# Optimization experiments

Measured on AMD Instinct MI355X. Metric: run time of the kernel, lower is better.

The kernel has to match this reference:

```python
import jax, jax.numpy as jnp
import numpy as np

N, E, F_IN, H, L = 50000, 800000, 128, 256, 3


def setup_inputs() -> dict:
    key = jax.random.key(0)
    ks = jax.random.split(key, 6)
    s = 0.05  # keep activations well-scaled through 3 residual layers
    return {
        "x": jax.random.normal(ks[0], (N, F_IN), jnp.float32),
        "edge_index": jax.random.randint(ks[1], (2, E), 0, N, dtype=jnp.int32),
        "Wp": jax.random.normal(ks[2], (H, F_IN), jnp.float32) * s,
        "bp": jnp.zeros((H,), jnp.float32),
        "Wl": jax.random.normal(ks[3], (L, H, H), jnp.float32) * s,
        "bl": jnp.zeros((L, H), jnp.float32),
        "Wr": jax.random.normal(ks[4], (L, H, H), jnp.float32) * s,
        "gamma": jnp.ones((L, H), jnp.float32),
        "beta": jnp.zeros((L, H), jnp.float32),
    }


def _layernorm(x, g, b, eps=1e-5):
    mu = jnp.mean(x, axis=-1, keepdims=True)
    var = jnp.var(x, axis=-1, keepdims=True)
    return (x - mu) * jax.lax.rsqrt(var + eps) * g + b


def reference(x, edge_index, Wp, bp, Wl, bl, Wr, gamma, beta):
    n = x.shape[0]
    src, dst = edge_index[0], edge_index[1]
    # input projection + ReLU
    h = jax.nn.relu(x @ Wp.T + bp)  # [N, H]
    # mean-aggregation normalizer (PyG SAGEConv 'mean'): zero-degree nodes -> 0
    deg = jax.ops.segment_sum(jnp.ones_like(dst, jnp.float32), dst, num_segments=n)
    inv_deg = (1.0 / jnp.maximum(deg, 1.0))[:, None]  # [N, 1]
    num_layers = Wl.shape[0]
    for i in range(num_layers):
        res = h
        # SAGEConv: lin_l(mean of source-neighbor messages) + lin_r(self)
        agg = jax.ops.segment_sum(h[src], dst, num_segments=n) * inv_deg  # [N, H]
        h = agg @ Wl[i].T + bl[i] + h @ Wr[i].T
        # LayerNorm -> ReLU -> (dropout: eval-mode identity) -> residual
        h = jax.nn.relu(_layernorm(h, gamma[i], beta[i])) + res
    return h
```

## Files before the change

### kernel.cpp

```cpp
#include <hip/hip_runtime.h>

#define NN 50000
#define EE 800000
#define FIN 128
#define HH 256
#define NL 3

#define BM 64
#define BK 32
#define ABYTES (BM*BK*2)
#define BBYTES (HH*BK*2)
#define TILEB  (ABYTES + BBYTES)

typedef __bf16 bf16x8 __attribute__((ext_vector_type(8)));
typedef float  f32x4  __attribute__((ext_vector_type(4)));
typedef unsigned short u16x8 __attribute__((ext_vector_type(8)));

__device__ __forceinline__ float bf2f(unsigned short u){
    union { unsigned int i; float f; } v; v.i = ((unsigned int)u) << 16; return v.f;
}
__device__ __forceinline__ unsigned short f2bf(float f){
    union { float f; unsigned int i; } v; v.f = f;
    unsigned int r = v.i + 0x7FFF + ((v.i >> 16) & 1);
    return (unsigned short)(r >> 16);
}
__device__ __forceinline__ void gload16(const void* g, void* s){
    __builtin_amdgcn_global_load_lds(
        (const __attribute__((address_space(1))) void*)g,
        (__attribute__((address_space(3))) void*)s, 16, 0, 0);
}

__global__ void k_zero_i32(int* __restrict__ p, int n){
    int i = blockIdx.x*256 + threadIdx.x;
    if (i < n) p[i] = 0;
}
__global__ void k_count_deg(const int* __restrict__ dst, int* __restrict__ deg){
    int i = blockIdx.x*256 + threadIdx.x;
    if (i < EE) atomicAdd(&deg[dst[i]], 1);
}
__global__ void k_block_sum(const int* __restrict__ deg, int* __restrict__ bsum){
    __shared__ int s[1024];
    int i = blockIdx.x*1024 + threadIdx.x;
    s[threadIdx.x] = (i < NN) ? deg[i] : 0;
    __syncthreads();
    for (int o = 512; o > 0; o >>= 1){
        if (threadIdx.x < o) s[threadIdx.x] += s[threadIdx.x + o];
        __syncthreads();
    }
    if (threadIdx.x == 0) bsum[blockIdx.x] = s[0];
}
__global__ void k_scan_bsum(int* __restrict__ bsum, int nb){
    if (threadIdx.x == 0 && blockIdx.x == 0){
        int run = 0;
        for (int i = 0; i < nb; ++i){ int v = bsum[i]; bsum[i] = run; run += v; }
    }
}
__global__ void k_make_off(const int* __restrict__ deg, const int* __restrict__ bsum,
                           int* __restrict__ off, int* __restrict__ pos,
                           float* __restrict__ invd){
    __shared__ int s[1024];
    int t = threadIdx.x;
    int i = blockIdx.x*1024 + t;
    int v = (i < NN) ? deg[i] : 0;
    s[t] = v; __syncthreads();
    for (int o = 1; o < 1024; o <<= 1){
        int add = (t >= o) ? s[t - o] : 0;
        __syncthreads();
        s[t] += add;
        __syncthreads();
    }
    if (i < NN){
        int excl = s[t] - v + bsum[blockIdx.x];
        off[i] = excl; pos[i] = excl;
        invd[i] = 1.0f / fmaxf((float)v, 1.0f);
    }
}
__global__ void k_build_csr(const int* __restrict__ src, const int* __restrict__ dst,
                            int* __restrict__ pos, int* __restrict__ csr){
    int i = blockIdx.x*256 + threadIdx.x;
    if (i < EE){
        int p = atomicAdd(&pos[dst[i]], 1);
        csr[p] = src[i];
    }
}

__global__ void k_cast4(const float* __restrict__ in, unsigned short* __restrict__ ob, int n4){
    int i = blockIdx.x*256 + threadIdx.x;
    if (i < n4){
        float4 v = *(const float4*)&in[i*4];
        ushort4 o; o.x=f2bf(v.x); o.y=f2bf(v.y); o.z=f2bf(v.z); o.w=f2bf(v.w);
        *(ushort4*)&ob[i*4] = o;
    }
}
__global__ void k_cast_wcat(const float* __restrict__ Wl, const float* __restrict__ Wr,
                            unsigned short* __restrict__ Wb){
    int i = blockIdx.x*256 + threadIdx.x;
    if (i < NL*HH*2*HH){
        int k = i & 511; int n = (i >> 9) & 255; int lyr = i >> 17;
        float v = (k < HH) ? Wl[((size_t)(lyr*HH)+n)*HH + k]
                           : Wr[((size_t)(lyr*HH)+n)*HH + (k-HH)];
        Wb[i] = f2bf(v);
    }
}

__global__ __launch_bounds__(256) void k_aggregate_bf(
    const unsigned short* __restrict__ hb, const int* __restrict__ csr,
    const int* __restrict__ off, const int* __restrict__ deg,
    const float* __restrict__ invd, unsigned short* __restrict__ aggb)
{
    const int wave = threadIdx.x >> 6, lane = threadIdx.x & 63;
    const int node = blockIdx.x*4 + wave;
    if (node >= NN) return;
    const int o = off[node], d = deg[node];
    const int half = lane >> 5;
    const int fl   = lane & 31;

    float acc[8] = {};
    int j = 0;
    for (; j + 8 <= d; j += 8){
        int s0 = csr[o + j     + half];
        int s1 = csr[o + j + 2 + half];
        int s2 = csr[o + j + 4 + half];
        int s3 = csr[o + j + 6 + half];
        u16x8 v0 = *(const u16x8*)&hb[(size_t)s0*HH + fl*8];
        u16x8 v1 = *(const u16x8*)&hb[(size_t)s1*HH + fl*8];
        u16x8 v2 = *(const u16x8*)&hb[(size_t)s2*HH + fl*8];
        u16x8 v3 = *(const u16x8*)&hb[(size_t)s3*HH + fl*8];
        #pragma unroll
        for (int k = 0; k < 8; ++k)
            acc[k] += (bf2f(v0[k]) + bf2f(v1[k])) + (bf2f(v2[k]) + bf2f(v3[k]));
    }
    for (; j < d; j += 2){
        int idx = j + half;
        if (idx < d){
            int s = csr[o + idx];
            u16x8 v = *(const u16x8*)&hb[(size_t)s*HH + fl*8];
            #pragma unroll
            for (int k = 0; k < 8; ++k) acc[k] += bf2f(v[k]);
        }
    }
    #pragma unroll
    for (int k = 0; k < 8; ++k) acc[k] += __shfl_xor(acc[k], 32);

    if (half == 0){
        float id = invd[node];
        u16x8 r;
        #pragma unroll
        for (int k = 0; k < 8; ++k) r[k] = f2bf(acc[k]*id);
        *(u16x8*)&aggb[(size_t)node*HH + fl*8] = r;
    }
}

template<int EPI>
__global__ __launch_bounds__(256) void k_gemm_mfma(
    const unsigned short* __restrict__ A0, int lda0,
    const unsigned short* __restrict__ A1, int lda1,
    const unsigned short* __restrict__ Bt,
    const float* __restrict__ bias,
    const float* __restrict__ gamma, const float* __restrict__ beta,
    const unsigned short* __restrict__ resb,
    float* __restrict__ outf, unsigned short* __restrict__ outb,
    int K0, int KTOT)
{
    __shared__ char smem[2*TILEB];
    const int t  = threadIdx.x;
    const int w  = t >> 6, l = t & 63;
    const int lr = l & 15, lg = l >> 4;
    const int m0 = blockIdx.x * BM;

    const int pA   = w*1024 + l*16;
    const int rowA = pA >> 6;
    const int swzA = (pA & 63) ^ ((rowA & 6) << 3);
    int growA = m0 + rowA; if (growA > NN-1) growA = NN-1;
    const char* a0base = (const char*)(A0 + (size_t)growA*lda0) + swzA;
    const char* a1base = (const char*)(A1 + (size_t)growA*lda1) + swzA;
    const char* bbase[4];
    #pragma unroll
    for (int c = 0; c < 4; ++c){
        int p = (w*4 + c)*1024 + l*16;
        int n = p >> 6;
        int swz = (p & 63) ^ ((n & 6) << 3);
        bbase[c] = (const char*)(Bt + (size_t)n*KTOT) + swz;
    }

    f32x4 acc[4][4] = {};

    auto stage = [&](int s, int buf){
        const int k0 = s * BK;
        char* dst = smem + buf*TILEB;
        const char* gA = (k0 < K0) ? (a0base + (size_t)k0*2)
                                   : (a1base + (size_t)(k0 - K0)*2);
        gload16(gA, dst + w*1024);
        #pragma unroll
        for (int c = 0; c < 4; ++c)
            gload16(bbase[c] + (size_t)k0*2, dst + ABYTES + (w*4 + c)*1024);
    };

    const int nsteps = KTOT / BK;
    stage(0, 0);
    for (int s = 0; s < nsteps; ++s){
        const int cur = s & 1;
        if (s + 1 < nsteps){
            stage(s + 1, cur ^ 1);
            asm volatile("s_waitcnt vmcnt(5)" ::: "memory");
        } else {
            asm volatile("s_waitcnt vmcnt(0)" ::: "memory");
        }
        __builtin_amdgcn_s_barrier();
        __builtin_amdgcn_sched_barrier(0);

        const char* As = smem + cur*TILEB;
        const char* Bs = As + ABYTES;
        const int kb = lg * 16;
        const int sw = (lr & 6) << 3;
        bf16x8 af[4], bfr[4];
        #pragma unroll
        for (int m = 0; m < 4; ++m){
            int r = m*16 + lr;
            af[m] = *(const bf16x8*)(As + r*64 + (kb ^ sw));
        }
        #pragma unroll
        for (int n = 0; n < 4; ++n){
            int r = w*64 + n*16 + lr;
            bfr[n] = *(const bf16x8*)(Bs + r*64 + (kb ^ sw));
        }
        #pragma unroll
        for (int m = 0; m < 4; ++m)
            #pragma unroll
            for (int n = 0; n < 4; ++n)
                acc[m][n] = __builtin_amdgcn_mfma_f32_16x16x32_bf16(af[m], bfr[n], acc[m][n], 0, 0, 0);

        asm volatile("s_waitcnt lgkmcnt(0)" ::: "memory");
        __builtin_amdgcn_s_barrier();
    }

    float bcol[4], gcol[4], becol[4];
    #pragma unroll
    for (int n = 0; n < 4; ++n){
        int c = w*64 + n*16 + lr;
        bcol[n] = bias[c];
        if (EPI >= 1){ gcol[n] = gamma[c]; becol[n] = beta[c]; }
    }

    if (EPI == 0){
        #pragma unroll
        for (int m = 0; m < 4; ++m)
        #pragma unroll
        for (int reg = 0; reg < 4; ++reg){
            int R = m*16 + lg*4 + reg;
            int grow = m0 + R;
            if (grow >= NN) continue;
            #pragma unroll
            for (int n = 0; n < 4; ++n){
                int c = w*64 + n*16 + lr;
                float v = fmaxf(acc[m][n][reg] + bcol[n], 0.f);
                outb[(size_t)grow*HH + c] = f2bf(v);
            }
        }
    } else {
        float sm[4][4], sq[4][4];
        #pragma unroll
        for (int m = 0; m < 4; ++m)
        #pragma unroll
        for (int reg = 0; reg < 4; ++reg){
            float s = 0.f, q = 0.f;
            #pragma unroll
            for (int n = 0; n < 4; ++n){
                float v = acc[m][n][reg] + bcol[n];
                acc[m][n][reg] = v;
                s += v; q += v*v;
            }
            sm[m][reg] = s; sq[m][reg] = q;
        }
        #pragma unroll
        for (int mask = 1; mask <= 8; mask <<= 1){
            #pragma unroll
            for (int m = 0; m < 4; ++m)
            #pragma unroll
            for (int reg = 0; reg < 4; ++reg){
                sm[m][reg] += __shfl_xor(sm[m][reg], mask);
                sq[m][reg] += __shfl_xor(sq[m][reg], mask);
            }
        }
        float* red = (float*)smem;
        __syncthreads();
        if (lr == 0){
            #pragma unroll
            for (int m = 0; m < 4; ++m)
            #pragma unroll
            for (int reg = 0; reg < 4; ++reg){
                int R = m*16 + lg*4 + reg;
                red[(w*64 + R)*2 + 0] = sm[m][reg];
                red[(w*64 + R)*2 + 1] = sq[m][reg];
            }
        }
        __syncthreads();
        #pragma unroll
        for (int m = 0; m < 4; ++m)
        #pragma unroll
        for (int reg = 0; reg < 4; ++reg){
            int R = m*16 + lg*4 + reg;
            float S = 0.f, Q = 0.f;
            #pragma unroll
            for (int ww = 0; ww < 4; ++ww){
                S += red[(ww*64 + R)*2 + 0];
                Q += red[(ww*64 + R)*2 + 1];
            }
            float mean = S * (1.0f/HH);
            float var  = Q * (1.0f/HH) - mean*mean;
            float inv  = rsqrtf(var + 1e-5f);
            int grow = m0 + R;
            if (grow >= NN) continue;
            #pragma unroll
            for (int n = 0; n < 4; ++n){
                int c = w*64 + n*16 + lr;
                float o = fmaxf((acc[m][n][reg] - mean)*inv*gcol[n] + becol[n], 0.f)
                          + bf2f(resb[(size_t)grow*HH + c]);
                if (EPI == 1) outb[(size_t)grow*HH + c] = f2bf(o);
                else          outf[(size_t)grow*HH + c] = o;
            }
        }
    }
}

extern "C" void kernel_launch(void* const* d_in, const int* in_sizes, int n_in,
                              void* d_out, int out_size, void* d_ws, size_t ws_size,
                              hipStream_t stream) {
    const float* x     = (const float*)d_in[0];
    const int*   ei    = (const int*)d_in[1];
    const int*   srcI  = ei;
    const int*   dstI  = ei + EE;
    const float* Wp    = (const float*)d_in[2];
    const float* bp    = (const float*)d_in[3];
    const float* Wl    = (const float*)d_in[4];
    const float* bl    = (const float*)d_in[5];
    const float* Wr    = (const float*)d_in[6];
    const float* gamma = (const float*)d_in[7];
    const float* beta  = (const float*)d_in[8];
    float* out = (float*)d_out;

    char* ws = (char*)d_ws;
    size_t off_b = 0;
    auto alloc = [&](size_t bytes) -> char* {
        char* p = ws + off_b;
        off_b = (off_b + bytes + 255) & ~(size_t)255;
        return p;
    };
    unsigned short* Hb0  = (unsigned short*)alloc((size_t)NN*HH*2);
    unsigned short* Hb1  = (unsigned short*)alloc((size_t)NN*HH*2);
    unsigned short* AGGb = (unsigned short*)alloc((size_t)NN*HH*2);
    unsigned short* Xb   = AGGb;
    int*   csr  = (int*)alloc((size_t)EE*4);
    int*   deg  = (int*)alloc((size_t)NN*4);
    int*   offs = (int*)alloc((size_t)NN*4);
    int*   pos  = (int*)alloc((size_t)NN*4);
    float* invd = (float*)alloc((size_t)NN*4);
    int*   bsum = (int*)alloc(64*4);
    unsigned short* Wpb = (unsigned short*)alloc((size_t)HH*FIN*2);
    unsigned short* Wb  = (unsigned short*)alloc((size_t)NL*HH*2*HH*2);
    (void)ws_size; (void)in_sizes; (void)n_in; (void)out_size;

    const int NB = (NN + 1023)/1024;

    k_zero_i32<<<(NN + 255)/256, 256, 0, stream>>>(deg, NN);
    k_count_deg<<<(EE + 255)/256, 256, 0, stream>>>(dstI, deg);
    k_block_sum<<<NB, 1024, 0, stream>>>(deg, bsum);
    k_scan_bsum<<<1, 1, 0, stream>>>(bsum, NB);
    k_make_off<<<NB, 1024, 0, stream>>>(deg, bsum, offs, pos, invd);
    k_build_csr<<<(EE + 255)/256, 256, 0, stream>>>(srcI, dstI, pos, csr);

    k_cast4<<<(NN*FIN/4 + 255)/256, 256, 0, stream>>>(x, Xb, NN*FIN/4);
    k_cast4<<<(HH*FIN/4 + 255)/256, 256, 0, stream>>>(Wp, Wpb, HH*FIN/4);
    k_cast_wcat<<<(NL*HH*2*HH + 255)/256, 256, 0, stream>>>(Wl, Wr, Wb);

    const int GB = (NN + BM - 1)/BM;

    k_gemm_mfma<0><<<GB, 256, 0, stream>>>(Xb, FIN, Xb, FIN, Wpb, bp,
                                           nullptr, nullptr, nullptr,
                                           nullptr, Hb0, FIN, FIN);

    unsigned short* hin = Hb0;
    for (int lyr = 0; lyr < NL; ++lyr){
        k_aggregate_bf<<<(NN + 3)/4, 256, 0, stream>>>(hin, csr, offs, deg, invd, AGGb);
        unsigned short* hout = (hin == Hb0) ? Hb1 : Hb0;
        const unsigned short* Wbt = Wb + (size_t)lyr*HH*2*HH;
        if (lyr < NL-1)
            k_gemm_mfma<1><<<GB, 256, 0, stream>>>(AGGb, HH, hin, HH, Wbt, bl + lyr*HH,
                                                   gamma + lyr*HH, beta + lyr*HH, hin,
                                                   nullptr, hout, HH, 2*HH);
        else
            k_gemm_mfma<2><<<GB, 256, 0, stream>>>(AGGb, HH, hin, HH, Wbt, bl + lyr*HH,
                                                   gamma + lyr*HH, beta + lyr*HH, hin,
                                                   out, nullptr, HH, 2*HH);
        hin = hout;
    }
}
```

Before: 421.1 us.

## Fuse neighbor mean-aggregation into the SAGE layer GEMM via shared memory

Removes the standalone aggregation kernel and computes the mean-aggregated rows for each 64-row tile directly inside the GEMM. The results are written into a swizzled LDS buffer that serves as the first half of the A operand. This avoids writing and re-reading the aggregated bf16 matrix in global memory for each layer and saves one launch per layer. In exchange, LDS use per block grows, which may lower occupancy. The latency-bound gather now runs with far fewer concurrent waves, each handling 16 nodes one after another.

New measurement: 570.1 us. 1.35x slower.

```diff
diff --git a/kernel.cpp b/kernel.cpp
--- a/kernel.cpp
+++ b/kernel.cpp
@@ -8,9 +8,6 @@
 
 #define BM 64
 #define BK 32
-#define ABYTES (BM*BK*2)
-#define BBYTES (HH*BK*2)
-#define TILEB  (ABYTES + BBYTES)
 
 typedef __bf16 bf16x8 __attribute__((ext_vector_type(8)));
 typedef float  f32x4  __attribute__((ext_vector_type(4)));
@@ -29,6 +26,9 @@
         (const __attribute__((address_space(1))) void*)g,
         (__attribute__((address_space(3))) void*)s, 16, 0, 0);
 }
+#define WAITV4 asm volatile("s_waitcnt vmcnt(4)" ::: "memory")
+#define WAITV5 asm volatile("s_waitcnt vmcnt(5)" ::: "memory")
+#define WAITV0 asm volatile("s_waitcnt vmcnt(0)" ::: "memory")
 
 __global__ void k_zero_i32(int* __restrict__ p, int n){
     int i = blockIdx.x*256 + threadIdx.x;
@@ -103,55 +103,7 @@
     }
 }
 
-__global__ __launch_bounds__(256) void k_aggregate_bf(
-    const unsigned short* __restrict__ hb, const int* __restrict__ csr,
-    const int* __restrict__ off, const int* __restrict__ deg,
-    const float* __restrict__ invd, unsigned short* __restrict__ aggb)
-{
-    const int wave = threadIdx.x >> 6, lane = threadIdx.x & 63;
-    const int node = blockIdx.x*4 + wave;
-    if (node >= NN) return;
-    const int o = off[node], d = deg[node];
-    const int half = lane >> 5;
-    const int fl   = lane & 31;
-
-    float acc[8] = {};
-    int j = 0;
-    for (; j + 8 <= d; j += 8){
-        int s0 = csr[o + j     + half];
-        int s1 = csr[o + j + 2 + half];
-        int s2 = csr[o + j + 4 + half];
-        int s3 = csr[o + j + 6 + half];
-        u16x8 v0 = *(const u16x8*)&hb[(size_t)s0*HH + fl*8];
-        u16x8 v1 = *(const u16x8*)&hb[(size_t)s1*HH + fl*8];
-        u16x8 v2 = *(const u16x8*)&hb[(size_t)s2*HH + fl*8];
-        u16x8 v3 = *(const u16x8*)&hb[(size_t)s3*HH + fl*8];
-        #pragma unroll
-        for (int k = 0; k < 8; ++k)
-            acc[k] += (bf2f(v0[k]) + bf2f(v1[k])) + (bf2f(v2[k]) + bf2f(v3[k]));
-    }
-    for (; j < d; j += 2){
-        int idx = j + half;
-        if (idx < d){
-            int s = csr[o + idx];
-            u16x8 v = *(const u16x8*)&hb[(size_t)s*HH + fl*8];
-            #pragma unroll
-            for (int k = 0; k < 8; ++k) acc[k] += bf2f(v[k]);
-        }
-    }
-    #pragma unroll
-    for (int k = 0; k < 8; ++k) acc[k] += __shfl_xor(acc[k], 32);
-
-    if (half == 0){
-        float id = invd[node];
-        u16x8 r;
-        #pragma unroll
-        for (int k = 0; k < 8; ++k) r[k] = f2bf(acc[k]*id);
-        *(u16x8*)&aggb[(size_t)node*HH + fl*8] = r;
-    }
-}
-
-template<int EPI>
+template<int EPI, int FUSE>
 __global__ __launch_bounds__(256) void k_gemm_mfma(
     const unsigned short* __restrict__ A0, int lda0,
     const unsigned short* __restrict__ A1, int lda1,
@@ -160,9 +112,15 @@
     const float* __restrict__ gamma, const float* __restrict__ beta,
     const unsigned short* __restrict__ resb,
     float* __restrict__ outf, unsigned short* __restrict__ outb,
+    const unsigned short* __restrict__ hb, const int* __restrict__ csr,
+    const int* __restrict__ offs, const int* __restrict__ deg,
+    const float* __restrict__ invd,
     int K0, int KTOT)
 {
-    __shared__ char smem[2*TILEB];
+    constexpr int A0SZ  = FUSE ? 32768 : 0;
+    constexpr int BOFF  = A0SZ;
+    constexpr int A1OFF = A0SZ + 2*16384;
+    __shared__ char smem[A1OFF + 2*4096];
     const int t  = threadIdx.x;
     const int w  = t >> 6, l = t & 63;
     const int lr = l & 15, lg = l >> 4;
@@ -187,30 +145,77 @@
 
     auto stage = [&](int s, int buf){
         const int k0 = s * BK;
-        char* dst = smem + buf*TILEB;
-        const char* gA = (k0 < K0) ? (a0base + (size_t)k0*2)
-                                   : (a1base + (size_t)(k0 - K0)*2);
-        gload16(gA, dst + w*1024);
         #pragma unroll
         for (int c = 0; c < 4; ++c)
-            gload16(bbase[c] + (size_t)k0*2, dst + ABYTES + (w*4 + c)*1024);
+            gload16(bbase[c] + (size_t)k0*2, smem + BOFF + buf*16384 + (w*4 + c)*1024);
+        if (!FUSE)
+            gload16(a0base + (size_t)k0*2, smem + A1OFF + buf*4096 + w*1024);
+        else if (k0 >= K0)
+            gload16(a1base + (size_t)(k0 - K0)*2, smem + A1OFF + buf*4096 + w*1024);
     };
 
+    stage(0, 0);
+
+    if (FUSE){
+        const int half = l >> 5;
+        const int fl   = l & 31;
+        for (int i = 0; i < 16; ++i){
+            int r = w*16 + i;
+            int node = m0 + r; if (node > NN-1) node = NN-1;
+            int o = offs[node], d = deg[node];
+            float a8[8] = {};
+            int j = 0;
+            for (; j + 8 <= d; j += 8){
+                int s0 = csr[o + j     + half];
+                int s1 = csr[o + j + 2 + half];
+                int s2 = csr[o + j + 4 + half];
+                int s3 = csr[o + j + 6 + half];
+                u16x8 v0 = *(const u16x8*)&hb[(size_t)s0*HH + fl*8];
+                u16x8 v1 = *(const u16x8*)&hb[(size_t)s1*HH + fl*8];
+                u16x8 v2 = *(const u16x8*)&hb[(size_t)s2*HH + fl*8];
+                u16x8 v3 = *(const u16x8*)&hb[(size_t)s3*HH + fl*8];
+                #pragma unroll
+                for (int k = 0; k < 8; ++k)
+                    a8[k] += (bf2f(v0[k]) + bf2f(v1[k])) + (bf2f(v2[k]) + bf2f(v3[k]));
+            }
+            for (; j < d; j += 2){
+                int idx = j + half;
+                if (idx < d){
+                    int s0 = csr[o + idx];
+                    u16x8 v0 = *(const u16x8*)&hb[(size_t)s0*HH + fl*8];
+                    #pragma unroll
+                    for (int k = 0; k < 8; ++k) a8[k] += bf2f(v0[k]);
+                }
+            }
+            #pragma unroll
+            for (int k = 0; k < 8; ++k) a8[k] += __shfl_xor(a8[k], 32);
+            if (half == 0){
+                float id = invd[node];
+                u16x8 rr;
+                #pragma unroll
+                for (int k = 0; k < 8; ++k) rr[k] = f2bf(a8[k]*id);
+                int ks = fl >> 2, q = fl & 3;
+                *(u16x8*)(smem + ks*4096 + r*64 + ((q*16) ^ ((r & 6) << 3))) = rr;
+            }
+        }
+        __syncthreads();
+    }
+
     const int nsteps = KTOT / BK;
-    stage(0, 0);
     for (int s = 0; s < nsteps; ++s){
         const int cur = s & 1;
         if (s + 1 < nsteps){
             stage(s + 1, cur ^ 1);
-            asm volatile("s_waitcnt vmcnt(5)" ::: "memory");
+            if (FUSE && (s + 1)*BK < K0) { WAITV4; } else { WAITV5; }
         } else {
-            asm volatile("s_waitcnt vmcnt(0)" ::: "memory");
+            WAITV0;
         }
         __builtin_amdgcn_s_barrier();
         __builtin_amdgcn_sched_barrier(0);
 
-        const char* As = smem + cur*TILEB;
-        const char* Bs = As + ABYTES;
+        const char* As = (FUSE && s*BK < K0) ? (smem + s*4096)
+                                             : (smem + A1OFF + cur*4096);
+        const char* Bs = smem + BOFF + cur*16384;
         const int kb = lg * 16;
         const int sw = (lr & 6) << 3;
         bf16x8 af[4], bfr[4];
@@ -346,10 +351,9 @@
         off_b = (off_b + bytes + 255) & ~(size_t)255;
         return p;
     };
-    unsigned short* Hb0  = (unsigned short*)alloc((size_t)NN*HH*2);
-    unsigned short* Hb1  = (unsigned short*)alloc((size_t)NN*HH*2);
-    unsigned short* AGGb = (unsigned short*)alloc((size_t)NN*HH*2);
-    unsigned short* Xb   = AGGb;
+    unsigned short* Hb0 = (unsigned short*)alloc((size_t)NN*HH*2);
+    unsigned short* Hb1 = (unsigned short*)alloc((size_t)NN*HH*2);
+    unsigned short* Xb  = (unsigned short*)alloc((size_t)NN*FIN*2);
     int*   csr  = (int*)alloc((size_t)EE*4);
     int*   deg  = (int*)alloc((size_t)NN*4);
     int*   offs = (int*)alloc((size_t)NN*4);
@@ -375,23 +379,28 @@
 
     const int GB = (NN + BM - 1)/BM;
 
-    k_gemm_mfma<0><<<GB, 256, 0, stream>>>(Xb, FIN, Xb, FIN, Wpb, bp,
-                                           nullptr, nullptr, nullptr,
-                                           nullptr, Hb0, FIN, FIN);
+    k_gemm_mfma<0,0><<<GB, 256, 0, stream>>>(Xb, FIN, Xb, FIN, Wpb, bp,
+                                             nullptr, nullptr, nullptr,
+                                             nullptr, Hb0,
+                                             nullptr, nullptr, nullptr, nullptr, nullptr,
+                                             FIN, FIN);
 
     unsigned short* hin = Hb0;
     for (int lyr = 0; lyr < NL; ++lyr){
-        k_aggregate_bf<<<(NN + 3)/4, 256, 0, stream>>>(hin, csr, offs, deg, invd, AGGb);
         unsigned short* hout = (hin == Hb0) ? Hb1 : Hb0;
         const unsigned short* Wbt = Wb + (size_t)lyr*HH*2*HH;
         if (lyr < NL-1)
-            k_gemm_mfma<1><<<GB, 256, 0, stream>>>(AGGb, HH, hin, HH, Wbt, bl + lyr*HH,
-                                                   gamma + lyr*HH, beta + lyr*HH, hin,
-                                                   nullptr, hout, HH, 2*HH);
+            k_gemm_mfma<1,1><<<GB, 256, 0, stream>>>(hin, HH, hin, HH, Wbt, bl + lyr*HH,
+                                                     gamma + lyr*HH, beta + lyr*HH, hin,
+                                                     nullptr, hout,
+                                                     hin, csr, offs, deg, invd,
+                                                     HH, 2*HH);
         else
-            k_gemm_mfma<2><<<GB, 256, 0, stream>>>(AGGb, HH, hin, HH, Wbt, bl + lyr*HH,
-                                                   gamma + lyr*HH, beta + lyr*HH, hin,
-                                                   out, nullptr, HH, 2*HH);
+            k_gemm_mfma<2,1><<<GB, 256, 0, stream>>>(hin, HH, hin, HH, Wbt, bl + lyr*HH,
+                                                     gamma + lyr*HH, beta + lyr*HH, hin,
+                                                     out, nullptr,
+                                                     hin, csr, offs, deg, invd,
+                                                     HH, 2*HH);
         hin = hout;
     }
 }
```

## Quantize hidden features to per-row uint8 for neighbor aggregation gathers

Applied to the files above, without the earlier changes.

The GEMM epilogues now also write each row of h as uint8 with a per-row max scale, and the aggregation kernel gathers these 1-byte values instead of bf16, halving the bytes per gathered neighbor row. The three casting kernels are merged into one prep launch. In exchange, the mean aggregation is computed from 8-bit quantized activations, which loses precision against the reference, and the epilogue gains an extra row-max reduction and byte stores.

After: 404.3 us. 1.04x faster.

```diff
diff --git a/kernel.cpp b/kernel.cpp
--- a/kernel.cpp
+++ b/kernel.cpp
@@ -84,70 +84,110 @@
     }
 }
 
-__global__ void k_cast4(const float* __restrict__ in, unsigned short* __restrict__ ob, int n4){
+#define NX  (NN*FIN/4)
+#define NWP (HH*FIN/4)
+#define NWC (NL*HH*2*HH/4)
+__global__ void k_prep(const float* __restrict__ x, const float* __restrict__ Wp,
+                       const float* __restrict__ Wl, const float* __restrict__ Wr,
+                       unsigned short* __restrict__ Xb, unsigned short* __restrict__ Wpb,
+                       unsigned short* __restrict__ Wb){
     int i = blockIdx.x*256 + threadIdx.x;
-    if (i < n4){
-        float4 v = *(const float4*)&in[i*4];
+    if (i < NX){
+        float4 v = *(const float4*)&x[i*4];
         ushort4 o; o.x=f2bf(v.x); o.y=f2bf(v.y); o.z=f2bf(v.z); o.w=f2bf(v.w);
-        *(ushort4*)&ob[i*4] = o;
-    }
-}
-__global__ void k_cast_wcat(const float* __restrict__ Wl, const float* __restrict__ Wr,
-                            unsigned short* __restrict__ Wb){
-    int i = blockIdx.x*256 + threadIdx.x;
-    if (i < NL*HH*2*HH){
-        int k = i & 511; int n = (i >> 9) & 255; int lyr = i >> 17;
-        float v = (k < HH) ? Wl[((size_t)(lyr*HH)+n)*HH + k]
-                           : Wr[((size_t)(lyr*HH)+n)*HH + (k-HH)];
-        Wb[i] = f2bf(v);
-    }
-}
-
-__global__ __launch_bounds__(256) void k_aggregate_bf(
-    const unsigned short* __restrict__ hb, const int* __restrict__ csr,
-    const int* __restrict__ off, const int* __restrict__ deg,
-    const float* __restrict__ invd, unsigned short* __restrict__ aggb)
+        *(ushort4*)&Xb[i*4] = o;
+        return;
+    }
+    int j = i - NX;
+    if (j < NWP){
+        float4 v = *(const float4*)&Wp[j*4];
+        ushort4 o; o.x=f2bf(v.x); o.y=f2bf(v.y); o.z=f2bf(v.z); o.w=f2bf(v.w);
+        *(ushort4*)&Wpb[j*4] = o;
+        return;
+    }
+    int k4 = j - NWP;
+    if (k4 < NWC){
+        int base = k4*4;
+        int kk  = base & 511;
+        int n   = (base >> 9) & (HH-1);
+        int lyr = base >> 17;
+        const float* srcp = (kk < HH) ? &Wl[((size_t)lyr*HH + n)*HH + kk]
+                                      : &Wr[((size_t)lyr*HH + n)*HH + (kk - HH)];
+        float4 v = *(const float4*)srcp;
+        ushort4 o; o.x=f2bf(v.x); o.y=f2bf(v.y); o.z=f2bf(v.z); o.w=f2bf(v.w);
+        *(ushort4*)&Wb[base] = o;
+    }
+}
+
+__device__ __forceinline__ void accum16(float* a, uint4 v, float c){
+    const unsigned int w0 = v.x, w1 = v.y, w2 = v.z, w3 = v.w;
+    #pragma unroll
+    for (int b = 0; b < 4; ++b){
+        a[b]    += c * (float)((w0 >> (8*b)) & 0xFF);
+        a[4+b]  += c * (float)((w1 >> (8*b)) & 0xFF);
+        a[8+b]  += c * (float)((w2 >> (8*b)) & 0xFF);
+        a[12+b] += c * (float)((w3 >> (8*b)) & 0xFF);
+    }
+}
+
+__global__ __launch_bounds__(256) void k_aggregate_u8(
+    const unsigned char* __restrict__ hu, const float* __restrict__ scl,
+    const int* __restrict__ csr, const int* __restrict__ off,
+    const int* __restrict__ deg, const float* __restrict__ invd,
+    unsigned short* __restrict__ aggb)
 {
     const int wave = threadIdx.x >> 6, lane = threadIdx.x & 63;
     const int node = blockIdx.x*4 + wave;
     if (node >= NN) return;
     const int o = off[node], d = deg[node];
-    const int half = lane >> 5;
-    const int fl   = lane & 31;
-
-    float acc[8] = {};
+    const int grp = lane >> 4;
+    const int fl  = lane & 15;
+
+    float acc[16] = {};
     int j = 0;
+    for (; j + 16 <= d; j += 16){
+        int s0 = csr[o + j      + grp];
+        int s1 = csr[o + j + 4  + grp];
+        int s2 = csr[o + j + 8  + grp];
+        int s3 = csr[o + j + 12 + grp];
+        float c0 = scl[s0], c1 = scl[s1], c2 = scl[s2], c3 = scl[s3];
+        uint4 v0 = *(const uint4*)&hu[(size_t)s0*HH + fl*16];
+        uint4 v1 = *(const uint4*)&hu[(size_t)s1*HH + fl*16];
+        uint4 v2 = *(const uint4*)&hu[(size_t)s2*HH + fl*16];
+        uint4 v3 = *(const uint4*)&hu[(size_t)s3*HH + fl*16];
+        accum16(acc, v0, c0); accum16(acc, v1, c1);
+        accum16(acc, v2, c2); accum16(acc, v3, c3);
+    }
     for (; j + 8 <= d; j += 8){
-        int s0 = csr[o + j     + half];
-        int s1 = csr[o + j + 2 + half];
-        int s2 = csr[o + j + 4 + half];
-        int s3 = csr[o + j + 6 + half];
-        u16x8 v0 = *(const u16x8*)&hb[(size_t)s0*HH + fl*8];
-        u16x8 v1 = *(const u16x8*)&hb[(size_t)s1*HH + fl*8];
-        u16x8 v2 = *(const u16x8*)&hb[(size_t)s2*HH + fl*8];
-        u16x8 v3 = *(const u16x8*)&hb[(size_t)s3*HH + fl*8];
-        #pragma unroll
-        for (int k = 0; k < 8; ++k)
-            acc[k] += (bf2f(v0[k]) + bf2f(v1[k])) + (bf2f(v2[k]) + bf2f(v3[k]));
-    }
-    for (; j < d; j += 2){
-        int idx = j + half;
-        if (idx < d){
-            int s = csr[o + idx];
-            u16x8 v = *(const u16x8*)&hb[(size_t)s*HH + fl*8];
-            #pragma unroll
-            for (int k = 0; k < 8; ++k) acc[k] += bf2f(v[k]);
-        }
+        int s0 = csr[o + j     + grp];
+        int s1 = csr[o + j + 4 + grp];
+        float c0 = scl[s0], c1 = scl[s1];
+        uint4 v0 = *(const uint4*)&hu[(size_t)s0*HH + fl*16];
+        uint4 v1 = *(const uint4*)&hu[(size_t)s1*HH + fl*16];
+        accum16(acc, v0, c0); accum16(acc, v1, c1);
+    }
+    for (; j < d; j += 4){
+        int idx = j + grp;
+        int s0 = 0; float c0 = 0.f;
+        if (idx < d){ s0 = csr[o + idx]; c0 = scl[s0]; }
+        uint4 v0 = *(const uint4*)&hu[(size_t)s0*HH + fl*16];
+        accum16(acc, v0, c0);
     }
     #pragma unroll
-    for (int k = 0; k < 8; ++k) acc[k] += __shfl_xor(acc[k], 32);
-
-    if (half == 0){
+    for (int k = 0; k < 16; ++k){
+        acc[k] += __shfl_xor(acc[k], 16);
+        acc[k] += __shfl_xor(acc[k], 32);
+    }
+    if (grp == 0){
         float id = invd[node];
-        u16x8 r;
-        #pragma unroll
-        for (int k = 0; k < 8; ++k) r[k] = f2bf(acc[k]*id);
-        *(u16x8*)&aggb[(size_t)node*HH + fl*8] = r;
+        u16x8 r0, r1;
+        #pragma unroll
+        for (int k = 0; k < 8; ++k){
+            r0[k] = f2bf(acc[k]*id);
+            r1[k] = f2bf(acc[8+k]*id);
+        }
+        *(u16x8*)&aggb[(size_t)node*HH + fl*16]     = r0;
+        *(u16x8*)&aggb[(size_t)node*HH + fl*16 + 8] = r1;
     }
 }
 
@@ -160,6 +200,7 @@
     const float* __restrict__ gamma, const float* __restrict__ beta,
     const unsigned short* __restrict__ resb,
     float* __restrict__ outf, unsigned short* __restrict__ outb,
+    unsigned char* __restrict__ hu, float* __restrict__ scl,
     int K0, int KTOT)
 {
     __shared__ char smem[2*TILEB];
@@ -242,6 +283,10 @@
         if (EPI >= 1){ gcol[n] = gamma[c]; becol[n] = beta[c]; }
     }
 
+    float* red  = (float*)smem;
+    float* red2 = red + 512;
+    float pmx[4][4];
+
     if (EPI == 0){
         #pragma unroll
         for (int m = 0; m < 4; ++m)
@@ -249,13 +294,16 @@
         for (int reg = 0; reg < 4; ++reg){
             int R = m*16 + lg*4 + reg;
             int grow = m0 + R;
-            if (grow >= NN) continue;
+            float mx = 0.f;
             #pragma unroll
             for (int n = 0; n < 4; ++n){
                 int c = w*64 + n*16 + lr;
                 float v = fmaxf(acc[m][n][reg] + bcol[n], 0.f);
-                outb[(size_t)grow*HH + c] = f2bf(v);
-            }
+                acc[m][n][reg] = v;
+                mx = fmaxf(mx, v);
+                if (grow < NN) outb[(size_t)grow*HH + c] = f2bf(v);
+            }
+            pmx[m][reg] = mx;
         }
     } else {
         float sm[4][4], sq[4][4];
@@ -282,7 +330,6 @@
                 sq[m][reg] += __shfl_xor(sq[m][reg], mask);
             }
         }
-        float* red = (float*)smem;
         __syncthreads();
         if (lr == 0){
             #pragma unroll
@@ -310,15 +357,59 @@
             float var  = Q * (1.0f/HH) - mean*mean;
             float inv  = rsqrtf(var + 1e-5f);
             int grow = m0 + R;
-            if (grow >= NN) continue;
+            float mx = 0.f;
             #pragma unroll
             for (int n = 0; n < 4; ++n){
                 int c = w*64 + n*16 + lr;
                 float o = fmaxf((acc[m][n][reg] - mean)*inv*gcol[n] + becol[n], 0.f)
                           + bf2f(resb[(size_t)grow*HH + c]);
-                if (EPI == 1) outb[(size_t)grow*HH + c] = f2bf(o);
-                else          outf[(size_t)grow*HH + c] = o;
-            }
+                acc[m][n][reg] = o;
+                mx = fmaxf(mx, o);
+                if (grow < NN){
+                    if (EPI == 1) outb[(size_t)grow*HH + c] = f2bf(o);
+                    else          outf[(size_t)grow*HH + c] = o;
+                }
+            }
+            pmx[m][reg] = mx;
+        }
+    }
+
+    if (EPI <= 1){
+        #pragma unroll
+        for (int mask = 1; mask <= 8; mask <<= 1){
+            #pragma unroll
+            for (int m = 0; m < 4; ++m)
+            #pragma unroll
+            for (int reg = 0; reg < 4; ++reg)
+                pmx[m][reg] = fmaxf(pmx[m][reg], __shfl_xor(pmx[m][reg], mask));
+        }
+        if (EPI == 0) __syncthreads();
+        if (lr == 0){
+            #pragma unroll
+            for (int m = 0; m < 4; ++m)
+            #pragma unroll
+            for (int reg = 0; reg < 4; ++reg){
+                int R = m*16 + lg*4 + reg;
+                red2[w*64 + R] = pmx[m][reg];
+            }
+        }
+        __syncthreads();
+        #pragma unroll
+        for (int m = 0; m < 4; ++m)
+        #pragma unroll
+        for (int reg = 0; reg < 4; ++reg){
+            int R = m*16 + lg*4 + reg;
+            float rmax = fmaxf(fmaxf(red2[R], red2[64 + R]),
+                               fmaxf(red2[128 + R], red2[192 + R]));
+            float qinv = (rmax > 0.f) ? (255.0f / rmax) : 0.f;
+            int grow = m0 + R;
+            if (grow >= NN) continue;
+            #pragma unroll
+            for (int n = 0; n < 4; ++n){
+                int c = w*64 + n*16 + lr;
+                hu[(size_t)grow*HH + c] = (unsigned char)(acc[m][n][reg]*qinv + 0.5f);
+            }
+            if (w == 0 && lr == 0) scl[grow] = rmax * (1.0f/255.0f);
         }
     }
 }
@@ -349,7 +440,11 @@
     unsigned short* Hb0  = (unsigned short*)alloc((size_t)NN*HH*2);
     unsigned short* Hb1  = (unsigned short*)alloc((size_t)NN*HH*2);
     unsigned short* AGGb = (unsigned short*)alloc((size_t)NN*HH*2);
-    unsigned short* Xb   = AGGb;
+    unsigned char*  Hu0  = (unsigned char*)alloc((size_t)NN*HH);
+    unsigned char*  Hu1  = (unsigned char*)alloc((size_t)NN*HH);
+    float* Scl0 = (float*)alloc((size_t)NN*4);
+    float* Scl1 = (float*)alloc((size_t)NN*4);
+    unsigned short* Xb = (unsigned short*)alloc((size_t)NN*FIN*2);
     int*   csr  = (int*)alloc((size_t)EE*4);
     int*   deg  = (int*)alloc((size_t)NN*4);
     int*   offs = (int*)alloc((size_t)NN*4);
@@ -369,29 +464,35 @@
     k_make_off<<<NB, 1024, 0, stream>>>(deg, bsum, offs, pos, invd);
     k_build_csr<<<(EE + 255)/256, 256, 0, stream>>>(srcI, dstI, pos, csr);
 
-    k_cast4<<<(NN*FIN/4 + 255)/256, 256, 0, stream>>>(x, Xb, NN*FIN/4);
-    k_cast4<<<(HH*FIN/4 + 255)/256, 256, 0, stream>>>(Wp, Wpb, HH*FIN/4);
-    k_cast_wcat<<<(NL*HH*2*HH + 255)/256, 256, 0, stream>>>(Wl, Wr, Wb);
+    k_prep<<<(NX + NWP + NWC + 255)/256, 256, 0, stream>>>(x, Wp, Wl, Wr, Xb, Wpb, Wb);
 
     const int GB = (NN + BM - 1)/BM;
 
     k_gemm_mfma<0><<<GB, 256, 0, stream>>>(Xb, FIN, Xb, FIN, Wpb, bp,
                                            nullptr, nullptr, nullptr,
-                                           nullptr, Hb0, FIN, FIN);
+                                           nullptr, Hb0, Hu0, Scl0,
+                                           FIN, FIN);
 
     unsigned short* hin = Hb0;
+    unsigned char*  huin = Hu0;
+    float*          sclin = Scl0;
     for (int lyr = 0; lyr < NL; ++lyr){
-        k_aggregate_bf<<<(NN + 3)/4, 256, 0, stream>>>(hin, csr, offs, deg, invd, AGGb);
-        unsigned short* hout = (hin == Hb0) ? Hb1 : Hb0;
+        k_aggregate_u8<<<(NN + 3)/4, 256, 0, stream>>>(huin, sclin, csr, offs, deg,
+                                                       invd, AGGb);
+        unsigned short* hout  = (hin == Hb0) ? Hb1 : Hb0;
+        unsigned char*  huout = (huin == Hu0) ? Hu1 : Hu0;
+        float*          sclout= (sclin == Scl0) ? Scl1 : Scl0;
         const unsigned short* Wbt = Wb + (size_t)lyr*HH*2*HH;
         if (lyr < NL-1)
             k_gemm_mfma<1><<<GB, 256, 0, stream>>>(AGGb, HH, hin, HH, Wbt, bl + lyr*HH,
                                                    gamma + lyr*HH, beta + lyr*HH, hin,
-                                                   nullptr, hout, HH, 2*HH);
+                                                   nullptr, hout, huout, sclout,
+                                                   HH, 2*HH);
         else
             k_gemm_mfma<2><<<GB, 256, 0, stream>>>(AGGb, HH, hin, HH, Wbt, bl + lyr*HH,
                                                    gamma + lyr*HH, beta + lyr*HH, hin,
-                                                   out, nullptr, HH, 2*HH);
-        hin = hout;
-    }
-}
+                                                   out, nullptr, nullptr, nullptr,
+                                                   HH, 2*HH);
+        hin = hout; huin = huout; sclin = sclout;
+    }
+}
```
